# Optimization experiments

Measured on AMD Instinct MI355X. Metric: run time of the kernel, lower is better.

Reference implementation:

```python
import jax, jax.numpy as jnp
import numpy as np

EMBED_DIM = 1024
N_HEADS = 16
HEAD_DIM = EMBED_DIM // N_HEADS
CHUNK = 64  # reward_data_gen_params['chunk_size']
B, T = 8, 1024


def setup_inputs() -> dict:
    key = jax.random.key(0)
    ks = jax.random.split(key, 9)
    s = 0.02
    return {
        "x": jax.random.normal(ks[0], (B, T, EMBED_DIM), dtype=jnp.float32),
        "Wq": jax.random.normal(ks[1], (EMBED_DIM, EMBED_DIM), dtype=jnp.float32) * s,
        "bq": jax.random.normal(ks[2], (EMBED_DIM,), dtype=jnp.float32) * s,
        "Wk": jax.random.normal(ks[3], (EMBED_DIM, EMBED_DIM), dtype=jnp.float32) * s,
        "bk": jax.random.normal(ks[4], (EMBED_DIM,), dtype=jnp.float32) * s,
        "Wv": jax.random.normal(ks[5], (EMBED_DIM, EMBED_DIM), dtype=jnp.float32) * s,
        "bv": jax.random.normal(ks[6], (EMBED_DIM,), dtype=jnp.float32) * s,
        "Wo": jax.random.normal(ks[7], (EMBED_DIM, EMBED_DIM), dtype=jnp.float32) * s,
        "bo": jax.random.normal(ks[8], (EMBED_DIM,), dtype=jnp.float32) * s,
        "attn_scale": jnp.full((1,), 1.0 / np.sqrt(HEAD_DIM), dtype=jnp.float32),
    }


def reference(x, Wq, bq, Wk, bk, Wv, bv, Wo, bo, attn_scale):
    Bsz, Tlen, C = x.shape
    H, D = N_HEADS, HEAD_DIM
    # torch Linear: y = x @ W.T + b
    q = (x @ Wq.T + bq).reshape(Bsz, Tlen, H, D).transpose(0, 2, 1, 3)  # [B,H,T,D]
    k = (x @ Wk.T + bk).reshape(Bsz, Tlen, H, D).transpose(0, 2, 1, 3)
    v = (x @ Wv.T + bv).reshape(Bsz, Tlen, H, D).transpose(0, 2, 1, 3)

    scores = jnp.einsum("bhqd,bhkd->bhqk", q, k) * attn_scale[0]  # [B,H,T,T]

    # Faithful reproduction of the chunked masking: the source only masks when
    # query-chunk >= key-chunk, which (given key>query implies key-chunk>=query-chunk)
    # reduces to masking key>query ONLY inside diagonal CHUNK x CHUNK blocks.
    idx = jnp.arange(Tlen)
    same_block = (idx[:, None] // CHUNK) == (idx[None, :] // CHUNK)
    mask = (idx[None, :] > idx[:, None]) & same_block  # [T,T] True => masked
    scores = jnp.where(mask[None, None], -jnp.inf, scores)

    w = jax.nn.softmax(scores, axis=-1)
    out = jnp.einsum("bhqk,bhkd->bhqd", w, v)  # [B,H,T,D]
    out = out.transpose(0, 2, 1, 3).reshape(Bsz, Tlen, C)
    return out @ Wo.T + bo
```

## Files before the change

kernel.cpp:

```cpp
#include <hip/hip_runtime.h>


typedef __bf16 bf16;
typedef __bf16 bf16x8 __attribute__((ext_vector_type(8)));
typedef float  f32x4  __attribute__((ext_vector_type(4)));

#define LOG2E 1.44269504088896340736f

__device__ __forceinline__ void async16(const bf16* g, bf16* l) {
  __builtin_amdgcn_global_load_lds(
      (const __attribute__((address_space(1))) void*)g,
      (__attribute__((address_space(3))) void*)l, 16, 0, 0);
}

#if __has_builtin(__builtin_amdgcn_exp2f)
#define EXP2F(x) __builtin_amdgcn_exp2f(x)
#else
#define EXP2F(x) exp2f(x)
#endif

__global__ __launch_bounds__(256) void k_convert(
    const float* __restrict__ x, const float* __restrict__ wq,
    const float* __restrict__ wk, const float* __restrict__ wv,
    const float* __restrict__ wo, bf16* __restrict__ xb, bf16* __restrict__ wb) {
  const int XV = (8192 * 1024) / 4;
  const int WV = (1024 * 1024) / 4;
  int i = blockIdx.x * 256 + threadIdx.x;
  const float4* src;
  bf16* dst;
  if (i < XV) {
    src = (const float4*)x + i;
    dst = xb + (size_t)i * 4;
  } else {
    int j = i - XV;
    int w = j / WV;
    int r = j - w * WV;
    const float* s = (w == 0) ? wq : (w == 1) ? wk : (w == 2) ? wv : wo;
    src = (const float4*)s + r;
    dst = wb + (size_t)w * (1024 * 1024) + (size_t)r * 4;
  }
  float4 f = *src;
  bf16 tmp[4] = {(bf16)f.x, (bf16)f.y, (bf16)f.z, (bf16)f.w};
  *(uint2*)dst = *(uint2*)tmp;
}

__global__ __launch_bounds__(256) void k_gemm_qkv(
    const bf16* __restrict__ A, const bf16* __restrict__ W,
    const float* __restrict__ bq, const float* __restrict__ bk,
    const float* __restrict__ bv, const float* __restrict__ scale_p,
    bf16* __restrict__ qb, bf16* __restrict__ kb, bf16* __restrict__ vb) {
  __shared__ __attribute__((aligned(16))) bf16 As[4096];
  __shared__ __attribute__((aligned(16))) bf16 Bs[4096];
  const int tid = threadIdx.x, lane = tid & 63, wid = tid >> 6;
  const int quad = lane >> 4, l16 = lane & 15;
  const int wm = (wid & 1) * 64, wn = (wid >> 1) * 64;
  const int tileM = blockIdx.x * 128, tileN = blockIdx.y * 128;

  const int rql = lane >> 2;
  const int lc = (lane & 3) ^ ((lane >> 3) & 3);
  const bf16* Ap = A + (size_t)(tileM + wid * 16 + rql) * 1024 + lc * 8;
  const bf16* Bp = W + (size_t)(tileN + wid * 16 + rql) * 1024 + lc * 8;
  bf16* AsW = As + wid * 512;
  bf16* BsW = Bs + wid * 512;

  f32x4 acc[4][4];
#pragma unroll
  for (int i = 0; i < 4; i++)
#pragma unroll
    for (int j = 0; j < 4; j++) acc[i][j] = (f32x4){0.f, 0.f, 0.f, 0.f};

  for (int k0 = 0; k0 < 1024; k0 += 32) {
    async16(Ap + k0, AsW);
    async16(Ap + k0 + 64 * 1024, AsW + 2048);
    async16(Bp + k0, BsW);
    async16(Bp + k0 + 64 * 1024, BsW + 2048);
    __syncthreads();
    bf16x8 af[4], bfr[4];
#pragma unroll
    for (int i = 0; i < 4; i++) {
      int r = wm + i * 16 + l16;
      af[i] = *(const bf16x8*)&As[r * 32 + ((quad ^ ((r >> 1) & 3)) * 8)];
    }
#pragma unroll
    for (int j = 0; j < 4; j++) {
      int r = wn + j * 16 + l16;
      bfr[j] = *(const bf16x8*)&Bs[r * 32 + ((quad ^ ((r >> 1) & 3)) * 8)];
    }
#pragma unroll
    for (int i = 0; i < 4; i++)
#pragma unroll
      for (int j = 0; j < 4; j++)
        acc[i][j] = __builtin_amdgcn_mfma_f32_16x16x32_bf16(af[i], bfr[j], acc[i][j], 0, 0, 0);
    __syncthreads();
  }

  float qscale = scale_p[0] * LOG2E;
#pragma unroll
  for (int i = 0; i < 4; i++) {
    int m0 = tileM + wm + i * 16 + quad * 4;
    int b = m0 >> 10;
    int t0 = m0 & 1023;
#pragma unroll
    for (int j = 0; j < 4; j++) {
      int n = tileN + wn + j * 16 + l16;
      int which = n >> 10;
      int nm = n & 1023;
      int h = nm >> 6, d = nm & 63;
      float bias = ((which == 0) ? bq : (which == 1) ? bk : bv)[nm];
      if (which == 2) {
        bf16 tmp[4];
#pragma unroll
        for (int r = 0; r < 4; r++) tmp[r] = (bf16)(acc[i][j][r] + bias);
        size_t vidx = (((size_t)((b * 16 + h) * 64 + d)) << 10) | (size_t)t0;
        *(uint2*)&vb[vidx] = *(uint2*)tmp;
      } else {
#pragma unroll
        for (int r = 0; r < 4; r++) {
          float v = acc[i][j][r] + bias;
          size_t idx = (((size_t)(b * 16 + h) * 1024 + (t0 + r)) << 6) | (size_t)d;
          if (which == 0) qb[idx] = (bf16)(v * qscale);
          else            kb[idx] = (bf16)v;
        }
      }
    }
  }
}

__global__ __launch_bounds__(256) void k_gemm_out(
    const bf16* __restrict__ A, const bf16* __restrict__ W,
    const float* __restrict__ bo, float* __restrict__ out) {
  __shared__ __attribute__((aligned(16))) bf16 As[4096];
  __shared__ __attribute__((aligned(16))) bf16 Bs[4096];
  const int tid = threadIdx.x, lane = tid & 63, wid = tid >> 6;
  const int quad = lane >> 4, l16 = lane & 15;
  const int wm = (wid & 1) * 64, wn = (wid >> 1) * 64;
  const int tileM = blockIdx.x * 128, tileN = blockIdx.y * 128;

  const int rql = lane >> 2;
  const int lc = (lane & 3) ^ ((lane >> 3) & 3);
  const bf16* Ap = A + (size_t)(tileM + wid * 16 + rql) * 1024 + lc * 8;
  const bf16* Bp = W + (size_t)(tileN + wid * 16 + rql) * 1024 + lc * 8;
  bf16* AsW = As + wid * 512;
  bf16* BsW = Bs + wid * 512;

  f32x4 acc[4][4];
#pragma unroll
  for (int i = 0; i < 4; i++)
#pragma unroll
    for (int j = 0; j < 4; j++) acc[i][j] = (f32x4){0.f, 0.f, 0.f, 0.f};

  for (int k0 = 0; k0 < 1024; k0 += 32) {
    async16(Ap + k0, AsW);
    async16(Ap + k0 + 64 * 1024, AsW + 2048);
    async16(Bp + k0, BsW);
    async16(Bp + k0 + 64 * 1024, BsW + 2048);
    __syncthreads();
    bf16x8 af[4], bfr[4];
#pragma unroll
    for (int i = 0; i < 4; i++) {
      int r = wm + i * 16 + l16;
      af[i] = *(const bf16x8*)&As[r * 32 + ((quad ^ ((r >> 1) & 3)) * 8)];
    }
#pragma unroll
    for (int j = 0; j < 4; j++) {
      int r = wn + j * 16 + l16;
      bfr[j] = *(const bf16x8*)&Bs[r * 32 + ((quad ^ ((r >> 1) & 3)) * 8)];
    }
#pragma unroll
    for (int i = 0; i < 4; i++)
#pragma unroll
      for (int j = 0; j < 4; j++)
        acc[i][j] = __builtin_amdgcn_mfma_f32_16x16x32_bf16(af[i], bfr[j], acc[i][j], 0, 0, 0);
    __syncthreads();
  }

#pragma unroll
  for (int i = 0; i < 4; i++)
#pragma unroll
    for (int j = 0; j < 4; j++) {
      int n = tileN + wn + j * 16 + l16;
      float bias = bo[n];
#pragma unroll
      for (int r = 0; r < 4; r++) {
        int m = tileM + wm + i * 16 + quad * 4 + r;
        out[(size_t)m * 1024 + n] = acc[i][j][r] + bias;
      }
    }
}

__global__ __launch_bounds__(256, 3) void k_attn(
    const bf16* __restrict__ qb, const bf16* __restrict__ kb,
    const bf16* __restrict__ vb, bf16* __restrict__ attn) {
  __shared__ __attribute__((aligned(16))) bf16 KsF[2][4096];
  __shared__ __attribute__((aligned(16))) bf16 VsF[2][4096];
  __shared__ __attribute__((aligned(16))) bf16 Pl[4][16][88];
  const int tid = threadIdx.x, lane = tid & 63, wid = tid >> 6;
  const int quad = lane >> 4, l16 = lane & 15;
  const int bh = blockIdx.x;
  const int qt2 = blockIdx.y;
  const size_t base = (size_t)bh * (1024 * 64);
  const int qrow0 = qt2 * 128;

  bf16x8 qf[2][2];
#pragma unroll
  for (int s = 0; s < 2; s++) {
    const bf16* qrow = qb + base + (size_t)(qrow0 + s * 64 + wid * 16 + l16) * 64;
    qf[s][0] = *(const bf16x8*)(qrow + quad * 8);
    qf[s][1] = *(const bf16x8*)(qrow + 32 + quad * 8);
  }

  f32x4 oacc[2][4], lacc[2];
#pragma unroll
  for (int s = 0; s < 2; s++) {
    lacc[s] = (f32x4){0.f, 0.f, 0.f, 0.f};
#pragma unroll
    for (int j = 0; j < 4; j++) oacc[s][j] = (f32x4){0.f, 0.f, 0.f, 0.f};
  }

  bf16x8 ones;
#pragma unroll
  for (int e = 0; e < 8; e++) ones[e] = (bf16)1.0f;

  const int krow = lane >> 3;
  const int klc = (lane & 7) ^ krow;
  const bf16* kp = kb + base + (size_t)(wid * 8 + krow) * 64 + klc * 8;
  const bf16* vp = vb + base + (size_t)(wid * 8 + krow) * 1024 + klc * 8;
  bf16* kd0[2] = {&KsF[0][wid * 512], &KsF[1][wid * 512]};
  bf16* vd0[2] = {&VsF[0][wid * 512], &VsF[1][wid * 512]};

  async16(kp, kd0[0]);
  async16(kp + 32 * 64, kd0[0] + 2048);
  async16(vp, vd0[0]);
  async16(vp + 32 * 1024, vd0[0] + 2048);

  for (int kt = 0; kt < 16; kt++) {
    const int pp = kt & 1;
    __syncthreads();

    if (kt < 15) {
      const bf16* kpn = kp + (size_t)(kt + 1) * 4096;
      const bf16* vpn = vp + (size_t)(kt + 1) * 64;
      async16(kpn, kd0[pp ^ 1]);
      async16(kpn + 32 * 64, kd0[pp ^ 1] + 2048);
      async16(vpn, vd0[pp ^ 1]);
      async16(vpn + 32 * 1024, vd0[pp ^ 1] + 2048);
    }

    const int sw = l16 & 7;
    bf16x8 kf[4][2], vf[2][4];
#pragma unroll
    for (int j = 0; j < 4; j++) {
      int row = (j * 16 + l16) * 64;
      kf[j][0] = *(const bf16x8*)&KsF[pp][row + ((quad ^ sw) * 8)];
      kf[j][1] = *(const bf16x8*)&KsF[pp][row + (((quad + 4) ^ sw) * 8)];
    }
#pragma unroll
    for (int ks = 0; ks < 2; ks++)
#pragma unroll
      for (int j = 0; j < 4; j++) {
        int row = (j * 16 + l16) * 64;
        vf[ks][j] = *(const bf16x8*)&VsF[pp][row + (((ks * 4 + quad) ^ sw) * 8)];
      }

#pragma unroll
    for (int s = 0; s < 2; s++) {
      f32x4 sv[4];
#pragma unroll
      for (int j = 0; j < 4; j++) {
        f32x4 z = (f32x4){0.f, 0.f, 0.f, 0.f};
        z = __builtin_amdgcn_mfma_f32_16x16x32_bf16(qf[s][0], kf[j][0], z, 0, 0, 0);
        z = __builtin_amdgcn_mfma_f32_16x16x32_bf16(qf[s][1], kf[j][1], z, 0, 0, 0);
        sv[j] = z;
      }
      if (qt2 * 2 + s == kt) {
#pragma unroll
        for (int j = 0; j < 4; j++) {
          int kpos = j * 16 + l16;
#pragma unroll
          for (int r = 0; r < 4; r++) {
            int qpos = wid * 16 + quad * 4 + r;
            if (kpos > qpos) sv[j][r] = -1e30f;
          }
        }
      }
#pragma unroll
      for (int j = 0; j < 4; j++)
#pragma unroll
        for (int r = 0; r < 4; r++)
          Pl[wid][quad * 4 + r][j * 16 + l16] = (bf16)EXP2F(sv[j][r]);
#pragma unroll
      for (int ks = 0; ks < 2; ks++) {
        bf16x8 pf = *(const bf16x8*)&Pl[wid][l16][ks * 32 + quad * 8];
#pragma unroll
        for (int j = 0; j < 4; j++)
          oacc[s][j] = __builtin_amdgcn_mfma_f32_16x16x32_bf16(pf, vf[ks][j], oacc[s][j], 0, 0, 0);
        lacc[s] = __builtin_amdgcn_mfma_f32_16x16x32_bf16(pf, ones, lacc[s], 0, 0, 0);
      }
    }
  }

  const int b = bh >> 4, h = bh & 15;
#pragma unroll
  for (int s = 0; s < 2; s++) {
    float inv[4];
#pragma unroll
    for (int r = 0; r < 4; r++) inv[r] = 1.0f / lacc[s][r];
#pragma unroll
    for (int j = 0; j < 4; j++)
#pragma unroll
      for (int r = 0; r < 4; r++) {
        int qg = qrow0 + s * 64 + wid * 16 + quad * 4 + r;
        float o = oacc[s][j][r] * inv[r];
        attn[((size_t)(b * 1024 + qg) << 10) + h * 64 + j * 16 + l16] = (bf16)o;
      }
  }
}

extern "C" void kernel_launch(void* const* d_in, const int* in_sizes, int n_in,
                              void* d_out, int out_size, void* d_ws, size_t ws_size,
                              hipStream_t stream) {
  const float* x     = (const float*)d_in[0];
  const float* Wq    = (const float*)d_in[1];
  const float* bq    = (const float*)d_in[2];
  const float* Wk    = (const float*)d_in[3];
  const float* bk    = (const float*)d_in[4];
  const float* Wv    = (const float*)d_in[5];
  const float* bv    = (const float*)d_in[6];
  const float* Wo    = (const float*)d_in[7];
  const float* bo    = (const float*)d_in[8];
  const float* scale = (const float*)d_in[9];

  char* ws = (char*)d_ws;
  bf16* xb   = (bf16*)(ws);
  bf16* wb   = (bf16*)(ws + (size_t)(16 << 20));
  bf16* qb   = (bf16*)(ws + (size_t)(24 << 20));
  bf16* kb   = (bf16*)(ws + (size_t)(40 << 20));
  bf16* vb   = (bf16*)(ws + (size_t)(56 << 20));
  bf16* attn = (bf16*)(ws + (size_t)(72 << 20));
  float* out = (float*)d_out;

  hipLaunchKernelGGL(k_convert, dim3(12288), dim3(256), 0, stream,
                     x, Wq, Wk, Wv, Wo, xb, wb);
  hipLaunchKernelGGL(k_gemm_qkv, dim3(64, 24), dim3(256), 0, stream,
                     xb, wb, bq, bk, bv, scale, qb, kb, vb);
  hipLaunchKernelGGL(k_attn, dim3(128, 8), dim3(256), 0, stream,
                     qb, kb, vb, attn);
  hipLaunchKernelGGL(k_gemm_out, dim3(64, 8), dim3(256), 0, stream,
                     attn, wb + (size_t)3072 * 1024, bo, out);
}
```

Measured before the change: 237.4 us.

## Double-buffer GEMM LDS tiles and widen attention query tile to 256 rows

Both GEMM kernels now use double-buffered LDS tiles with a prefetch of the next K-slice issued after a single barrier per iteration, so global loads can overlap MFMA work instead of stalling on two barriers per step. The attention kernel processes 256 query rows per block instead of 128, which halves how often each K/V tile is loaded. P tiles for all four sub-tiles are staged in LDS and V fragments are loaded once per k-slice, with occupancy lowered from 3 to 2 blocks per CU. The attention output now reuses the bf16 x workspace buffer, and the convert kernel uses shifts instead of division; the larger tile adds register and LDS pressure.

```diff
diff --git a/kernel.cpp b/kernel.cpp
--- a/kernel.cpp
+++ b/kernel.cpp
@@ -33,8 +33,8 @@
     dst = xb + (size_t)i * 4;
   } else {
     int j = i - XV;
-    int w = j / WV;
-    int r = j - w * WV;
+    int w = j >> 18;
+    int r = j & (WV - 1);
     const float* s = (w == 0) ? wq : (w == 1) ? wk : (w == 2) ? wv : wo;
     src = (const float4*)s + r;
     dst = wb + (size_t)w * (1024 * 1024) + (size_t)r * 4;
@@ -49,8 +49,8 @@
     const float* __restrict__ bq, const float* __restrict__ bk,
     const float* __restrict__ bv, const float* __restrict__ scale_p,
     bf16* __restrict__ qb, bf16* __restrict__ kb, bf16* __restrict__ vb) {
-  __shared__ __attribute__((aligned(16))) bf16 As[4096];
-  __shared__ __attribute__((aligned(16))) bf16 Bs[4096];
+  __shared__ __attribute__((aligned(16))) bf16 As[2][4096];
+  __shared__ __attribute__((aligned(16))) bf16 Bs[2][4096];
   const int tid = threadIdx.x, lane = tid & 63, wid = tid >> 6;
   const int quad = lane >> 4, l16 = lane & 15;
   const int wm = (wid & 1) * 64, wn = (wid >> 1) * 64;
@@ -60,8 +60,7 @@
   const int lc = (lane & 3) ^ ((lane >> 3) & 3);
   const bf16* Ap = A + (size_t)(tileM + wid * 16 + rql) * 1024 + lc * 8;
   const bf16* Bp = W + (size_t)(tileN + wid * 16 + rql) * 1024 + lc * 8;
-  bf16* AsW = As + wid * 512;
-  bf16* BsW = Bs + wid * 512;
+  const int wofs = wid * 512;
 
   f32x4 acc[4][4];
 #pragma unroll
@@ -69,29 +68,37 @@
 #pragma unroll
     for (int j = 0; j < 4; j++) acc[i][j] = (f32x4){0.f, 0.f, 0.f, 0.f};
 
-  for (int k0 = 0; k0 < 1024; k0 += 32) {
-    async16(Ap + k0, AsW);
-    async16(Ap + k0 + 64 * 1024, AsW + 2048);
-    async16(Bp + k0, BsW);
-    async16(Bp + k0 + 64 * 1024, BsW + 2048);
+  async16(Ap, &As[0][wofs]);
+  async16(Ap + 64 * 1024, &As[0][2048 + wofs]);
+  async16(Bp, &Bs[0][wofs]);
+  async16(Bp + 64 * 1024, &Bs[0][2048 + wofs]);
+
+  for (int it = 0; it < 32; it++) {
+    const int pp = it & 1;
     __syncthreads();
+    if (it < 31) {
+      int k0 = (it + 1) * 32;
+      async16(Ap + k0, &As[pp ^ 1][wofs]);
+      async16(Ap + k0 + 64 * 1024, &As[pp ^ 1][2048 + wofs]);
+      async16(Bp + k0, &Bs[pp ^ 1][wofs]);
+      async16(Bp + k0 + 64 * 1024, &Bs[pp ^ 1][2048 + wofs]);
+    }
     bf16x8 af[4], bfr[4];
 #pragma unroll
     for (int i = 0; i < 4; i++) {
       int r = wm + i * 16 + l16;
-      af[i] = *(const bf16x8*)&As[r * 32 + ((quad ^ ((r >> 1) & 3)) * 8)];
+      af[i] = *(const bf16x8*)&As[pp][r * 32 + ((quad ^ ((r >> 1) & 3)) * 8)];
     }
 #pragma unroll
     for (int j = 0; j < 4; j++) {
       int r = wn + j * 16 + l16;
-      bfr[j] = *(const bf16x8*)&Bs[r * 32 + ((quad ^ ((r >> 1) & 3)) * 8)];
+      bfr[j] = *(const bf16x8*)&Bs[pp][r * 32 + ((quad ^ ((r >> 1) & 3)) * 8)];
     }
 #pragma unroll
     for (int i = 0; i < 4; i++)
 #pragma unroll
       for (int j = 0; j < 4; j++)
         acc[i][j] = __builtin_amdgcn_mfma_f32_16x16x32_bf16(af[i], bfr[j], acc[i][j], 0, 0, 0);
-    __syncthreads();
   }
 
   float qscale = scale_p[0] * LOG2E;
@@ -129,8 +136,8 @@
 __global__ __launch_bounds__(256) void k_gemm_out(
     const bf16* __restrict__ A, const bf16* __restrict__ W,
     const float* __restrict__ bo, float* __restrict__ out) {
-  __shared__ __attribute__((aligned(16))) bf16 As[4096];
-  __shared__ __attribute__((aligned(16))) bf16 Bs[4096];
+  __shared__ __attribute__((aligned(16))) bf16 As[2][4096];
+  __shared__ __attribute__((aligned(16))) bf16 Bs[2][4096];
   const int tid = threadIdx.x, lane = tid & 63, wid = tid >> 6;
   const int quad = lane >> 4, l16 = lane & 15;
   const int wm = (wid & 1) * 64, wn = (wid >> 1) * 64;
@@ -140,8 +147,7 @@
   const int lc = (lane & 3) ^ ((lane >> 3) & 3);
   const bf16* Ap = A + (size_t)(tileM + wid * 16 + rql) * 1024 + lc * 8;
   const bf16* Bp = W + (size_t)(tileN + wid * 16 + rql) * 1024 + lc * 8;
-  bf16* AsW = As + wid * 512;
-  bf16* BsW = Bs + wid * 512;
+  const int wofs = wid * 512;
 
   f32x4 acc[4][4];
 #pragma unroll
@@ -149,29 +155,37 @@
 #pragma unroll
     for (int j = 0; j < 4; j++) acc[i][j] = (f32x4){0.f, 0.f, 0.f, 0.f};
 
-  for (int k0 = 0; k0 < 1024; k0 += 32) {
-    async16(Ap + k0, AsW);
-    async16(Ap + k0 + 64 * 1024, AsW + 2048);
-    async16(Bp + k0, BsW);
-    async16(Bp + k0 + 64 * 1024, BsW + 2048);
+  async16(Ap, &As[0][wofs]);
+  async16(Ap + 64 * 1024, &As[0][2048 + wofs]);
+  async16(Bp, &Bs[0][wofs]);
+  async16(Bp + 64 * 1024, &Bs[0][2048 + wofs]);
+
+  for (int it = 0; it < 32; it++) {
+    const int pp = it & 1;
     __syncthreads();
+    if (it < 31) {
+      int k0 = (it + 1) * 32;
+      async16(Ap + k0, &As[pp ^ 1][wofs]);
+      async16(Ap + k0 + 64 * 1024, &As[pp ^ 1][2048 + wofs]);
+      async16(Bp + k0, &Bs[pp ^ 1][wofs]);
+      async16(Bp + k0 + 64 * 1024, &Bs[pp ^ 1][2048 + wofs]);
+    }
     bf16x8 af[4], bfr[4];
 #pragma unroll
     for (int i = 0; i < 4; i++) {
       int r = wm + i * 16 + l16;
-      af[i] = *(const bf16x8*)&As[r * 32 + ((quad ^ ((r >> 1) & 3)) * 8)];
+      af[i] = *(const bf16x8*)&As[pp][r * 32 + ((quad ^ ((r >> 1) & 3)) * 8)];
     }
 #pragma unroll
     for (int j = 0; j < 4; j++) {
       int r = wn + j * 16 + l16;
-      bfr[j] = *(const bf16x8*)&Bs[r * 32 + ((quad ^ ((r >> 1) & 3)) * 8)];
+      bfr[j] = *(const bf16x8*)&Bs[pp][r * 32 + ((quad ^ ((r >> 1) & 3)) * 8)];
     }
 #pragma unroll
     for (int i = 0; i < 4; i++)
 #pragma unroll
       for (int j = 0; j < 4; j++)
         acc[i][j] = __builtin_amdgcn_mfma_f32_16x16x32_bf16(af[i], bfr[j], acc[i][j], 0, 0, 0);
-    __syncthreads();
   }
 
 #pragma unroll
@@ -188,30 +202,30 @@
     }
 }
 
-__global__ __launch_bounds__(256, 3) void k_attn(
+__global__ __launch_bounds__(256, 2) void k_attn(
     const bf16* __restrict__ qb, const bf16* __restrict__ kb,
     const bf16* __restrict__ vb, bf16* __restrict__ attn) {
   __shared__ __attribute__((aligned(16))) bf16 KsF[2][4096];
   __shared__ __attribute__((aligned(16))) bf16 VsF[2][4096];
-  __shared__ __attribute__((aligned(16))) bf16 Pl[4][16][88];
+  __shared__ __attribute__((aligned(16))) bf16 Pl[4][4][16][72];
   const int tid = threadIdx.x, lane = tid & 63, wid = tid >> 6;
   const int quad = lane >> 4, l16 = lane & 15;
   const int bh = blockIdx.x;
-  const int qt2 = blockIdx.y;
+  const int qt = blockIdx.y;
   const size_t base = (size_t)bh * (1024 * 64);
-  const int qrow0 = qt2 * 128;
-
-  bf16x8 qf[2][2];
-#pragma unroll
-  for (int s = 0; s < 2; s++) {
+  const int qrow0 = qt * 256;
+
+  bf16x8 qf[4][2];
+#pragma unroll
+  for (int s = 0; s < 4; s++) {
     const bf16* qrow = qb + base + (size_t)(qrow0 + s * 64 + wid * 16 + l16) * 64;
     qf[s][0] = *(const bf16x8*)(qrow + quad * 8);
     qf[s][1] = *(const bf16x8*)(qrow + 32 + quad * 8);
   }
 
-  f32x4 oacc[2][4], lacc[2];
-#pragma unroll
-  for (int s = 0; s < 2; s++) {
+  f32x4 oacc[4][4], lacc[4];
+#pragma unroll
+  for (int s = 0; s < 4; s++) {
     lacc[s] = (f32x4){0.f, 0.f, 0.f, 0.f};
 #pragma unroll
     for (int j = 0; j < 4; j++) oacc[s][j] = (f32x4){0.f, 0.f, 0.f, 0.f};
@@ -225,14 +239,14 @@
   const int klc = (lane & 7) ^ krow;
   const bf16* kp = kb + base + (size_t)(wid * 8 + krow) * 64 + klc * 8;
   const bf16* vp = vb + base + (size_t)(wid * 8 + krow) * 1024 + klc * 8;
-  bf16* kd0[2] = {&KsF[0][wid * 512], &KsF[1][wid * 512]};
-  bf16* vd0[2] = {&VsF[0][wid * 512], &VsF[1][wid * 512]};
-
-  async16(kp, kd0[0]);
-  async16(kp + 32 * 64, kd0[0] + 2048);
-  async16(vp, vd0[0]);
-  async16(vp + 32 * 1024, vd0[0] + 2048);
-
+  const int wofs = wid * 512;
+
+  async16(kp, &KsF[0][wofs]);
+  async16(kp + 32 * 64, &KsF[0][2048 + wofs]);
+  async16(vp, &VsF[0][wofs]);
+  async16(vp + 32 * 1024, &VsF[0][2048 + wofs]);
+
+  const int sw = l16 & 7;
   for (int kt = 0; kt < 16; kt++) {
     const int pp = kt & 1;
     __syncthreads();
@@ -240,14 +254,13 @@
     if (kt < 15) {
       const bf16* kpn = kp + (size_t)(kt + 1) * 4096;
       const bf16* vpn = vp + (size_t)(kt + 1) * 64;
-      async16(kpn, kd0[pp ^ 1]);
-      async16(kpn + 32 * 64, kd0[pp ^ 1] + 2048);
-      async16(vpn, vd0[pp ^ 1]);
-      async16(vpn + 32 * 1024, vd0[pp ^ 1] + 2048);
-    }
-
-    const int sw = l16 & 7;
-    bf16x8 kf[4][2], vf[2][4];
+      async16(kpn, &KsF[pp ^ 1][wofs]);
+      async16(kpn + 32 * 64, &KsF[pp ^ 1][2048 + wofs]);
+      async16(vpn, &VsF[pp ^ 1][wofs]);
+      async16(vpn + 32 * 1024, &VsF[pp ^ 1][2048 + wofs]);
+    }
+
+    bf16x8 kf[4][2];
 #pragma unroll
     for (int j = 0; j < 4; j++) {
       int row = (j * 16 + l16) * 64;
@@ -255,15 +268,7 @@
       kf[j][1] = *(const bf16x8*)&KsF[pp][row + (((quad + 4) ^ sw) * 8)];
     }
 #pragma unroll
-    for (int ks = 0; ks < 2; ks++)
-#pragma unroll
-      for (int j = 0; j < 4; j++) {
-        int row = (j * 16 + l16) * 64;
-        vf[ks][j] = *(const bf16x8*)&VsF[pp][row + (((ks * 4 + quad) ^ sw) * 8)];
-      }
-
-#pragma unroll
-    for (int s = 0; s < 2; s++) {
+    for (int s = 0; s < 4; s++) {
       f32x4 sv[4];
 #pragma unroll
       for (int j = 0; j < 4; j++) {
@@ -272,7 +277,7 @@
         z = __builtin_amdgcn_mfma_f32_16x16x32_bf16(qf[s][1], kf[j][1], z, 0, 0, 0);
         sv[j] = z;
       }
-      if (qt2 * 2 + s == kt) {
+      if (qt * 4 + s == kt) {
 #pragma unroll
         for (int j = 0; j < 4; j++) {
           int kpos = j * 16 + l16;
@@ -287,13 +292,23 @@
       for (int j = 0; j < 4; j++)
 #pragma unroll
         for (int r = 0; r < 4; r++)
-          Pl[wid][quad * 4 + r][j * 16 + l16] = (bf16)EXP2F(sv[j][r]);
-#pragma unroll
-      for (int ks = 0; ks < 2; ks++) {
-        bf16x8 pf = *(const bf16x8*)&Pl[wid][l16][ks * 32 + quad * 8];
+          Pl[wid][s][quad * 4 + r][j * 16 + l16] = (bf16)EXP2F(sv[j][r]);
+    }
+
+#pragma unroll
+    for (int ks = 0; ks < 2; ks++) {
+      bf16x8 vf[4];
+#pragma unroll
+      for (int j = 0; j < 4; j++) {
+        int row = (j * 16 + l16) * 64;
+        vf[j] = *(const bf16x8*)&VsF[pp][row + (((ks * 4 + quad) ^ sw) * 8)];
+      }
+#pragma unroll
+      for (int s = 0; s < 4; s++) {
+        bf16x8 pf = *(const bf16x8*)&Pl[wid][s][l16][ks * 32 + quad * 8];
 #pragma unroll
         for (int j = 0; j < 4; j++)
-          oacc[s][j] = __builtin_amdgcn_mfma_f32_16x16x32_bf16(pf, vf[ks][j], oacc[s][j], 0, 0, 0);
+          oacc[s][j] = __builtin_amdgcn_mfma_f32_16x16x32_bf16(pf, vf[j], oacc[s][j], 0, 0, 0);
         lacc[s] = __builtin_amdgcn_mfma_f32_16x16x32_bf16(pf, ones, lacc[s], 0, 0, 0);
       }
     }
@@ -301,7 +316,7 @@
 
   const int b = bh >> 4, h = bh & 15;
 #pragma unroll
-  for (int s = 0; s < 2; s++) {
+  for (int s = 0; s < 4; s++) {
     float inv[4];
 #pragma unroll
     for (int r = 0; r < 4; r++) inv[r] = 1.0f / lacc[s][r];
@@ -336,14 +351,14 @@
   bf16* qb   = (bf16*)(ws + (size_t)(24 << 20));
   bf16* kb   = (bf16*)(ws + (size_t)(40 << 20));
   bf16* vb   = (bf16*)(ws + (size_t)(56 << 20));
-  bf16* attn = (bf16*)(ws + (size_t)(72 << 20));
+  bf16* attn = xb;
   float* out = (float*)d_out;
 
   hipLaunchKernelGGL(k_convert, dim3(12288), dim3(256), 0, stream,
                      x, Wq, Wk, Wv, Wo, xb, wb);
   hipLaunchKernelGGL(k_gemm_qkv, dim3(64, 24), dim3(256), 0, stream,
                      xb, wb, bq, bk, bv, scale, qb, kb, vb);
-  hipLaunchKernelGGL(k_attn, dim3(128, 8), dim3(256), 0, stream,
+  hipLaunchKernelGGL(k_attn, dim3(128, 4), dim3(256), 0, stream,
                      qb, kb, vb, attn);
   hipLaunchKernelGGL(k_gemm_out, dim3(64, 8), dim3(256), 0, stream,
                      attn, wb + (size_t)3072 * 1024, bo, out);
```

New measurement: 252.6 us. 6.4% more time.
